# Performance work log

Hardware: AMD Instinct MI355X
Metric: run time of the kernel (lower is better)

## Reference

```python
import jax, jax.numpy as jnp
import numpy as np

EMB_DIM = 1024
HEAD_SIZE = 64
SEQ = 2048
BATCH = 8


def setup_inputs() -> dict:
    key = jax.random.key(0)
    kx, kq, kk, kv = jax.random.split(key, 4)
    x = jax.random.normal(kx, (BATCH, SEQ, EMB_DIM), dtype=jnp.float32)
    # nn.Linear(E, H, bias=False): y = x @ W.T with W of shape [H, E]; store as [E, H]
    s = 1.0 / np.sqrt(EMB_DIM)
    Wq = jax.random.uniform(kq, (EMB_DIM, HEAD_SIZE), jnp.float32, -s, s)
    Wk = jax.random.uniform(kk, (EMB_DIM, HEAD_SIZE), jnp.float32, -s, s)
    Wv = jax.random.uniform(kv, (EMB_DIM, HEAD_SIZE), jnp.float32, -s, s)
    return {"x": x, "Wq": Wq, "Wk": Wk, "Wv": Wv}


def reference(x, Wq, Wk, Wv):
    B, S, E = x.shape
    q = jnp.einsum("bse,eh->bsh", x, Wq)
    k = jnp.einsum("bse,eh->bsh", x, Wk)
    v = jnp.einsum("bse,eh->bsh", x, Wv)
    # NOTE: original scales by E**-0.5 (embedding dim), not head_size**-0.5
    att = jnp.einsum("bqh,bkh->bqk", q, k) * (E ** -0.5)
    causal = jnp.tril(jnp.ones((S, S), dtype=bool))
    att = jnp.where(causal, att, -jnp.inf)
    att = jax.nn.softmax(att, axis=-1)
    # dropout(p=0.2) treated as identity (eval mode) for deterministic reference
    out = jnp.einsum("bqk,bkh->bqh", att, v)
    return out
```

## Files before the change

kernel.cpp:

```cpp
#include <hip/hip_runtime.h>

constexpr int Bn = 8, S = 2048, E = 1024, H = 64;
constexpr float SCALE = 0.03125f;
constexpr float LOG2E = 1.44269504f;

typedef __attribute__((ext_vector_type(8))) short short8;
typedef __attribute__((ext_vector_type(4))) float f32x4;

__device__ __forceinline__ unsigned short f2bf(float f) {
  unsigned u = __builtin_bit_cast(unsigned, f);
  u += 0x7fffu + ((u >> 16) & 1u);
  return (unsigned short)(u >> 16);
}
__device__ __forceinline__ ushort4 f4bf(float4 f) {
  return make_ushort4(f2bf(f.x), f2bf(f.y), f2bf(f.z), f2bf(f.w));
}

__global__ __launch_bounds__(256) void wtrans_kernel(
    const float* __restrict__ Wq, const float* __restrict__ Wk,
    const float* __restrict__ Wv, unsigned short* __restrict__ WT3) {
  __shared__ unsigned short tb[64][72];
  const int m = blockIdx.x >> 4;
  const int e0 = (blockIdx.x & 15) * 64;
  const float* W = (m == 0) ? Wq : (m == 1) ? Wk : Wv;
  const int t = threadIdx.x;
#pragma unroll
  for (int it = 0; it < 4; ++it) {
    int idx = t + it * 256;
    int r = idx >> 4, c4 = idx & 15;
    float4 f = ((const float4*)(W + (long)(e0 + r) * H))[c4];
    *(ushort4*)&tb[r][c4 * 4] = f4bf(f);
  }
  __syncthreads();
#pragma unroll
  for (int it = 0; it < 4; ++it) {
    int idx = t + it * 256;
    int h = idx >> 4, e4 = idx & 15;
    ushort4 u = make_ushort4(tb[e4 * 4 + 0][h], tb[e4 * 4 + 1][h],
                             tb[e4 * 4 + 2][h], tb[e4 * 4 + 3][h]);
    ((ushort4*)(WT3 + (long)(m * 64 + h) * E + e0))[e4] = u;
  }
}

__global__ __launch_bounds__(256) void qkv_kernel(
    const float* __restrict__ x, const unsigned short* __restrict__ WT3,
    unsigned short* __restrict__ q, unsigned short* __restrict__ kk,
    unsigned short* __restrict__ vT) {
  __shared__ unsigned short xs[32][136];
  __shared__ unsigned short ws[192][136];
  const int t = threadIdx.x;
  const int w = t >> 6, lane = t & 63, l15 = lane & 15, g = lane >> 4;
  const long row0 = (long)blockIdx.x * 32;
  const int xrow = t >> 5, xslot = t & 31;
  const int wrow = t >> 4, wslot = t & 15;

  f32x4 acc[2][3];
#pragma unroll
  for (int rt = 0; rt < 2; ++rt)
#pragma unroll
    for (int ct = 0; ct < 3; ++ct) acc[rt][ct] = f32x4{0.f, 0.f, 0.f, 0.f};

  float4 px[4];
  short8 pw[12];
#pragma unroll
  for (int it = 0; it < 4; ++it)
    px[it] = ((const float4*)(x + (row0 + xrow + it * 8) * E))[xslot];
#pragma unroll
  for (int it = 0; it < 12; ++it)
    pw[it] = *(const short8*)(WT3 + (long)(wrow + it * 16) * E + wslot * 8);
#pragma unroll
  for (int it = 0; it < 4; ++it)
    *(ushort4*)&xs[xrow + it * 8][xslot * 4] = f4bf(px[it]);
#pragma unroll
  for (int it = 0; it < 12; ++it)
    *(short8*)&ws[wrow + it * 16][wslot * 8] = pw[it];

  for (int c = 0; c < 8; ++c) {
    __syncthreads();
    if (c < 7) {
      const int e0 = (c + 1) * 128;
#pragma unroll
      for (int it = 0; it < 4; ++it)
        px[it] = ((const float4*)(x + (row0 + xrow + it * 8) * E + e0))[xslot];
#pragma unroll
      for (int it = 0; it < 12; ++it)
        pw[it] = *(const short8*)(WT3 + (long)(wrow + it * 16) * E + e0 + wslot * 8);
    }
#pragma unroll
    for (int kh = 0; kh < 4; ++kh) {
      short8 a0 = *(const short8*)&xs[l15][kh * 32 + g * 8];
      short8 a1 = *(const short8*)&xs[16 + l15][kh * 32 + g * 8];
#pragma unroll
      for (int ct = 0; ct < 3; ++ct) {
        short8 b = *(const short8*)&ws[w * 48 + ct * 16 + l15][kh * 32 + g * 8];
        acc[0][ct] = __builtin_amdgcn_mfma_f32_16x16x32_bf16(a0, b, acc[0][ct], 0, 0, 0);
        acc[1][ct] = __builtin_amdgcn_mfma_f32_16x16x32_bf16(a1, b, acc[1][ct], 0, 0, 0);
      }
    }
    __syncthreads();
    if (c < 7) {
#pragma unroll
      for (int it = 0; it < 4; ++it)
        *(ushort4*)&xs[xrow + it * 8][xslot * 4] = f4bf(px[it]);
#pragma unroll
      for (int it = 0; it < 12; ++it)
        *(short8*)&ws[wrow + it * 16][wslot * 8] = pw[it];
    }
  }

  const int bb = (int)(row0 >> 11);
  const int srow = (int)(row0 & 2047);
#pragma unroll
  for (int ct = 0; ct < 3; ++ct) {
    const int col = w * 48 + ct * 16 + l15;
    const int mm = col >> 6, ch = col & 63;
#pragma unroll
    for (int rt = 0; rt < 2; ++rt) {
      const int srl = rt * 16 + g * 4;
      if (mm == 0) {
#pragma unroll
        for (int r = 0; r < 4; ++r)
          q[(row0 + srl + r) * H + ch] = f2bf(acc[rt][ct][r] * SCALE);
      } else if (mm == 1) {
#pragma unroll
        for (int r = 0; r < 4; ++r)
          kk[(row0 + srl + r) * H + ch] = f2bf(acc[rt][ct][r]);
      } else {
        ushort4 v4 = make_ushort4(f2bf(acc[rt][ct][0]), f2bf(acc[rt][ct][1]),
                                  f2bf(acc[rt][ct][2]), f2bf(acc[rt][ct][3]));
        *(ushort4*)(vT + ((long)bb * H + ch) * S + srow + srl) = v4;
      }
    }
  }
}

__global__ __launch_bounds__(256, 2) void attn_kernel(
    const unsigned short* __restrict__ q, const unsigned short* __restrict__ k,
    const unsigned short* __restrict__ vT, float* __restrict__ out) {
  __shared__ unsigned short pl[4][16][72];
  __shared__ float Om[2][64][20];
  __shared__ float ms[2][16], ls[2][16];
  const int t = threadIdx.x;
  const int w = t >> 6, lane = t & 63, l15 = lane & 15, g = lane >> 4;
  const int b = blockIdx.x & 7, p = blockIdx.x >> 3;
  const int grp = w >> 1, sp = w & 1;
  const int qt = grp ? (127 - p) : p;
  const int qrow0 = qt * 16;
  const int nt = (16 * qt + 79) >> 6;
  const unsigned short* kb = k + (long)b * S * H;
  const unsigned short* vb = vT + (long)b * H * S;
  const unsigned short* qp = q + ((long)b * S + qrow0 + l15) * H + g * 8;
  short8 bq0 = *(const short8*)qp;
  short8 bq1 = *(const short8*)(qp + 32);

  f32x4 O[4];
#pragma unroll
  for (int c = 0; c < 4; ++c) O[c] = f32x4{0.f, 0.f, 0.f, 0.f};
  float m_ = -1e30f, l_ = 0.f;

  short8 ak[4][2];
  int kt = sp;
  if (kt < nt) {
#pragma unroll
    for (int c = 0; c < 4; ++c)
#pragma unroll
      for (int kh = 0; kh < 2; ++kh)
        ak[c][kh] = *(const short8*)(kb + (long)(kt * 64 + c * 16 + l15) * H + kh * 32 + g * 8);
  }

  for (; kt < nt; kt += 2) {
    short8 av[4][2];
#pragma unroll
    for (int c = 0; c < 4; ++c)
#pragma unroll
      for (int kh = 0; kh < 2; ++kh)
        av[c][kh] = *(const short8*)(vb + (long)(c * 16 + l15) * S + kt * 64 + kh * 32 + g * 8);
    f32x4 sc[4];
#pragma unroll
    for (int c = 0; c < 4; ++c) {
      sc[c] = f32x4{0.f, 0.f, 0.f, 0.f};
      sc[c] = __builtin_amdgcn_mfma_f32_16x16x32_bf16(ak[c][0], bq0, sc[c], 0, 0, 0);
      sc[c] = __builtin_amdgcn_mfma_f32_16x16x32_bf16(ak[c][1], bq1, sc[c], 0, 0, 0);
    }
    if (kt + 2 < nt) {
#pragma unroll
      for (int c = 0; c < 4; ++c)
#pragma unroll
        for (int kh = 0; kh < 2; ++kh)
          ak[c][kh] = *(const short8*)(kb + (long)((kt + 2) * 64 + c * 16 + l15) * H + kh * 32 + g * 8);
    }
    if (kt == nt - 1) {
#pragma unroll
      for (int c = 0; c < 4; ++c)
#pragma unroll
        for (int r = 0; r < 4; ++r)
          if (kt * 64 + c * 16 + g * 4 + r > qrow0 + l15) sc[c][r] = -1e30f;
    }
    float mx = -1e30f;
#pragma unroll
    for (int c = 0; c < 4; ++c)
#pragma unroll
      for (int r = 0; r < 4; ++r) mx = fmaxf(mx, sc[c][r]);
    mx = fmaxf(mx, __shfl_xor(mx, 16));
    mx = fmaxf(mx, __shfl_xor(mx, 32));
    float mn = fmaxf(m_, mx);
    float al = exp2f((m_ - mn) * LOG2E);
    float sum = 0.f;
#pragma unroll
    for (int c = 0; c < 4; ++c)
#pragma unroll
      for (int r = 0; r < 4; ++r) {
        float pe = exp2f((sc[c][r] - mn) * LOG2E);
        sc[c][r] = pe;
        sum += pe;
      }
    sum += __shfl_xor(sum, 16);
    sum += __shfl_xor(sum, 32);
    l_ = l_ * al + sum;
    m_ = mn;
#pragma unroll
    for (int c = 0; c < 4; ++c) {
      ushort4 p4 = make_ushort4(f2bf(sc[c][0]), f2bf(sc[c][1]),
                                f2bf(sc[c][2]), f2bf(sc[c][3]));
      *(ushort4*)&pl[w][l15][c * 16 + g * 4] = p4;
    }
#pragma unroll
    for (int c = 0; c < 4; ++c)
#pragma unroll
      for (int r = 0; r < 4; ++r) O[c][r] *= al;
    short8 bp0 = *(const short8*)&pl[w][l15][g * 8];
    short8 bp1 = *(const short8*)&pl[w][l15][32 + g * 8];
#pragma unroll
    for (int c = 0; c < 4; ++c) {
      O[c] = __builtin_amdgcn_mfma_f32_16x16x32_bf16(av[c][0], bp0, O[c], 0, 0, 0);
      O[c] = __builtin_amdgcn_mfma_f32_16x16x32_bf16(av[c][1], bp1, O[c], 0, 0, 0);
    }
  }

  if (sp == 1) {
#pragma unroll
    for (int c = 0; c < 4; ++c)
#pragma unroll
      for (int r = 0; r < 4; ++r)
        Om[grp][c * 16 + g * 4 + r][l15] = O[c][r];
    if (g == 0) { ms[grp][l15] = m_; ls[grp][l15] = l_; }
  }
  __syncthreads();
  if (sp == 0) {
    float m1 = ms[grp][l15], l1 = ls[grp][l15];
    float mstar = fmaxf(m_, m1);
    float f0 = exp2f((m_ - mstar) * LOG2E);
    float f1 = exp2f((m1 - mstar) * LOG2E);
    float inv = 1.0f / (l_ * f0 + l1 * f1);
    float* op = out + ((long)b * S + qrow0 + l15) * H;
#pragma unroll
    for (int c = 0; c < 4; ++c) {
      float4 o;
      o.x = (O[c][0] * f0 + Om[grp][c * 16 + g * 4 + 0][l15] * f1) * inv;
      o.y = (O[c][1] * f0 + Om[grp][c * 16 + g * 4 + 1][l15] * f1) * inv;
      o.z = (O[c][2] * f0 + Om[grp][c * 16 + g * 4 + 2][l15] * f1) * inv;
      o.w = (O[c][3] * f0 + Om[grp][c * 16 + g * 4 + 3][l15] * f1) * inv;
      *(float4*)(op + c * 16 + g * 4) = o;
    }
  }
}

extern "C" void kernel_launch(void* const* d_in, const int* in_sizes, int n_in,
                              void* d_out, int out_size, void* d_ws, size_t ws_size,
                              hipStream_t stream) {
  const float* x  = (const float*)d_in[0];
  const float* Wq = (const float*)d_in[1];
  const float* Wk = (const float*)d_in[2];
  const float* Wv = (const float*)d_in[3];
  float* outp = (float*)d_out;
  unsigned short* WT3 = (unsigned short*)d_ws;
  unsigned short* q  = (unsigned short*)((char*)d_ws + 512 * 1024);
  unsigned short* kk = q + (size_t)Bn * S * H;
  unsigned short* vT = kk + (size_t)Bn * S * H;
  wtrans_kernel<<<dim3(48), dim3(256), 0, stream>>>(Wq, Wk, Wv, WT3);
  qkv_kernel<<<dim3((Bn * S) / 32), dim3(256), 0, stream>>>(x, WT3, q, kk, vT);
  attn_kernel<<<dim3(Bn * 64), dim3(256), 0, stream>>>(q, kk, vT, outp);
}
```

Before: 141.3 us.

## Split each attention block's key range across all four waves for both query tiles

Previously each block paired a short and a long query tile, with two waves per tile splitting key tiles in stride 2. Now all four waves process both query tiles in turn, striding key tiles by 4 with a rotated start offset so that work stays balanced across waves. The four partial softmax states are merged through larger shared-memory buffers. LOG2E is also folded into the Q scale so exp2 skips a multiply. This adds shared-memory traffic and a four-way merge, and keeps two sets of accumulators live, which raises register pressure.

```diff
diff --git a/kernel.cpp b/kernel.cpp
--- a/kernel.cpp
+++ b/kernel.cpp
@@ -1,8 +1,7 @@
 #include <hip/hip_runtime.h>
 
 constexpr int Bn = 8, S = 2048, E = 1024, H = 64;
-constexpr float SCALE = 0.03125f;
-constexpr float LOG2E = 1.44269504f;
+constexpr float SCALE = 0.03125f * 1.44269504f;
 
 typedef __attribute__((ext_vector_type(8))) short short8;
 typedef __attribute__((ext_vector_type(4))) float f32x4;
@@ -138,129 +137,148 @@
     const unsigned short* __restrict__ q, const unsigned short* __restrict__ k,
     const unsigned short* __restrict__ vT, float* __restrict__ out) {
   __shared__ unsigned short pl[4][16][72];
-  __shared__ float Om[2][64][20];
-  __shared__ float ms[2][16], ls[2][16];
+  __shared__ float Om[2][4][64][17];
+  __shared__ float ms[2][4][16], ls[2][4][16];
   const int t = threadIdx.x;
   const int w = t >> 6, lane = t & 63, l15 = lane & 15, g = lane >> 4;
   const int b = blockIdx.x & 7, p = blockIdx.x >> 3;
-  const int grp = w >> 1, sp = w & 1;
-  const int qt = grp ? (127 - p) : p;
-  const int qrow0 = qt * 16;
-  const int nt = (16 * qt + 79) >> 6;
   const unsigned short* kb = k + (long)b * S * H;
   const unsigned short* vb = vT + (long)b * H * S;
-  const unsigned short* qp = q + ((long)b * S + qrow0 + l15) * H + g * 8;
-  short8 bq0 = *(const short8*)qp;
-  short8 bq1 = *(const short8*)(qp + 32);
-
-  f32x4 O[4];
-#pragma unroll
-  for (int c = 0; c < 4; ++c) O[c] = f32x4{0.f, 0.f, 0.f, 0.f};
-  float m_ = -1e30f, l_ = 0.f;
-
-  short8 ak[4][2];
-  int kt = sp;
-  if (kt < nt) {
+
+  const int qt0 = p, qt1 = 127 - p;
+  const int nt0 = (qt0 >> 2) + 1;
+  const int nt1 = (qt1 >> 2) + 1;
+  const int qtA[2] = {qt0, qt1};
+  const int ntA[2] = {nt0, nt1};
+  const int k0A[2] = {w, (w + 4 - (nt0 & 3)) & 3};
+
+  short8 bq0[2], bq1[2];
+  f32x4 O[2][4];
+  float m_[2], l_[2];
+#pragma unroll
+  for (int ph = 0; ph < 2; ++ph) {
+    const unsigned short* qp = q + ((long)b * S + qtA[ph] * 16 + l15) * H + g * 8;
+    bq0[ph] = *(const short8*)qp;
+    bq1[ph] = *(const short8*)(qp + 32);
+    m_[ph] = -1e30f;
+    l_[ph] = 0.f;
+#pragma unroll
+    for (int c = 0; c < 4; ++c) O[ph][c] = f32x4{0.f, 0.f, 0.f, 0.f};
+  }
+
+#pragma unroll
+  for (int ph = 0; ph < 2; ++ph) {
+    const int qrow0 = qtA[ph] * 16;
+    const int ntp = ntA[ph];
+    short8 ak[4][2];
+    int kt = k0A[ph];
+    if (kt < ntp) {
+#pragma unroll
+      for (int c = 0; c < 4; ++c)
+#pragma unroll
+        for (int kh = 0; kh < 2; ++kh)
+          ak[c][kh] = *(const short8*)(kb + (long)(kt * 64 + c * 16 + l15) * H + kh * 32 + g * 8);
+    }
+    for (; kt < ntp; kt += 4) {
+      short8 av[4][2];
+#pragma unroll
+      for (int c = 0; c < 4; ++c)
+#pragma unroll
+        for (int kh = 0; kh < 2; ++kh)
+          av[c][kh] = *(const short8*)(vb + (long)(c * 16 + l15) * S + kt * 64 + kh * 32 + g * 8);
+      f32x4 sc[4];
+#pragma unroll
+      for (int c = 0; c < 4; ++c) {
+        sc[c] = f32x4{0.f, 0.f, 0.f, 0.f};
+        sc[c] = __builtin_amdgcn_mfma_f32_16x16x32_bf16(ak[c][0], bq0[ph], sc[c], 0, 0, 0);
+        sc[c] = __builtin_amdgcn_mfma_f32_16x16x32_bf16(ak[c][1], bq1[ph], sc[c], 0, 0, 0);
+      }
+      if (kt + 4 < ntp) {
+#pragma unroll
+        for (int c = 0; c < 4; ++c)
+#pragma unroll
+          for (int kh = 0; kh < 2; ++kh)
+            ak[c][kh] = *(const short8*)(kb + (long)((kt + 4) * 64 + c * 16 + l15) * H + kh * 32 + g * 8);
+      }
+      if (kt == ntp - 1) {
+#pragma unroll
+        for (int c = 0; c < 4; ++c)
+#pragma unroll
+          for (int r = 0; r < 4; ++r)
+            if (kt * 64 + c * 16 + g * 4 + r > qrow0 + l15) sc[c][r] = -1e30f;
+      }
+      float mx = -1e30f;
+#pragma unroll
+      for (int c = 0; c < 4; ++c)
+#pragma unroll
+        for (int r = 0; r < 4; ++r) mx = fmaxf(mx, sc[c][r]);
+      mx = fmaxf(mx, __shfl_xor(mx, 16));
+      mx = fmaxf(mx, __shfl_xor(mx, 32));
+      float mn = fmaxf(m_[ph], mx);
+      float al = exp2f(m_[ph] - mn);
+      float sum = 0.f;
+#pragma unroll
+      for (int c = 0; c < 4; ++c)
+#pragma unroll
+        for (int r = 0; r < 4; ++r) {
+          float pe = exp2f(sc[c][r] - mn);
+          sc[c][r] = pe;
+          sum += pe;
+        }
+      sum += __shfl_xor(sum, 16);
+      sum += __shfl_xor(sum, 32);
+      l_[ph] = l_[ph] * al + sum;
+      m_[ph] = mn;
+#pragma unroll
+      for (int c = 0; c < 4; ++c) {
+        ushort4 p4 = make_ushort4(f2bf(sc[c][0]), f2bf(sc[c][1]),
+                                  f2bf(sc[c][2]), f2bf(sc[c][3]));
+        *(ushort4*)&pl[w][l15][c * 16 + g * 4] = p4;
+      }
+#pragma unroll
+      for (int c = 0; c < 4; ++c)
+#pragma unroll
+        for (int r = 0; r < 4; ++r) O[ph][c][r] *= al;
+      short8 bp0 = *(const short8*)&pl[w][l15][g * 8];
+      short8 bp1 = *(const short8*)&pl[w][l15][32 + g * 8];
+#pragma unroll
+      for (int c = 0; c < 4; ++c) {
+        O[ph][c] = __builtin_amdgcn_mfma_f32_16x16x32_bf16(av[c][0], bp0, O[ph][c], 0, 0, 0);
+        O[ph][c] = __builtin_amdgcn_mfma_f32_16x16x32_bf16(av[c][1], bp1, O[ph][c], 0, 0, 0);
+      }
+    }
+  }
+
+#pragma unroll
+  for (int ph = 0; ph < 2; ++ph) {
 #pragma unroll
     for (int c = 0; c < 4; ++c)
 #pragma unroll
-      for (int kh = 0; kh < 2; ++kh)
-        ak[c][kh] = *(const short8*)(kb + (long)(kt * 64 + c * 16 + l15) * H + kh * 32 + g * 8);
-  }
-
-  for (; kt < nt; kt += 2) {
-    short8 av[4][2];
-#pragma unroll
-    for (int c = 0; c < 4; ++c)
-#pragma unroll
-      for (int kh = 0; kh < 2; ++kh)
-        av[c][kh] = *(const short8*)(vb + (long)(c * 16 + l15) * S + kt * 64 + kh * 32 + g * 8);
-    f32x4 sc[4];
+      for (int r = 0; r < 4; ++r)
+        Om[ph][w][c * 16 + g * 4 + r][l15] = O[ph][c][r];
+    if (g == 0) { ms[ph][w][l15] = m_[ph]; ls[ph][w][l15] = l_[ph]; }
+  }
+  __syncthreads();
+  if (w < 2) {
+    const int ph = w;
+    float mm0 = ms[ph][0][l15], mm1 = ms[ph][1][l15];
+    float mm2 = ms[ph][2][l15], mm3 = ms[ph][3][l15];
+    float mstar = fmaxf(fmaxf(mm0, mm1), fmaxf(mm2, mm3));
+    float f0 = exp2f(mm0 - mstar), f1 = exp2f(mm1 - mstar);
+    float f2 = exp2f(mm2 - mstar), f3 = exp2f(mm3 - mstar);
+    float inv = 1.0f / (ls[ph][0][l15] * f0 + ls[ph][1][l15] * f1 +
+                        ls[ph][2][l15] * f2 + ls[ph][3][l15] * f3);
+    float* op = out + ((long)b * S + qtA[ph] * 16 + l15) * H;
 #pragma unroll
     for (int c = 0; c < 4; ++c) {
-      sc[c] = f32x4{0.f, 0.f, 0.f, 0.f};
-      sc[c] = __builtin_amdgcn_mfma_f32_16x16x32_bf16(ak[c][0], bq0, sc[c], 0, 0, 0);
-      sc[c] = __builtin_amdgcn_mfma_f32_16x16x32_bf16(ak[c][1], bq1, sc[c], 0, 0, 0);
-    }
-    if (kt + 2 < nt) {
-#pragma unroll
-      for (int c = 0; c < 4; ++c)
-#pragma unroll
-        for (int kh = 0; kh < 2; ++kh)
-          ak[c][kh] = *(const short8*)(kb + (long)((kt + 2) * 64 + c * 16 + l15) * H + kh * 32 + g * 8);
-    }
-    if (kt == nt - 1) {
-#pragma unroll
-      for (int c = 0; c < 4; ++c)
-#pragma unroll
-        for (int r = 0; r < 4; ++r)
-          if (kt * 64 + c * 16 + g * 4 + r > qrow0 + l15) sc[c][r] = -1e30f;
-    }
-    float mx = -1e30f;
-#pragma unroll
-    for (int c = 0; c < 4; ++c)
-#pragma unroll
-      for (int r = 0; r < 4; ++r) mx = fmaxf(mx, sc[c][r]);
-    mx = fmaxf(mx, __shfl_xor(mx, 16));
-    mx = fmaxf(mx, __shfl_xor(mx, 32));
-    float mn = fmaxf(m_, mx);
-    float al = exp2f((m_ - mn) * LOG2E);
-    float sum = 0.f;
-#pragma unroll
-    for (int c = 0; c < 4; ++c)
+      float o4[4];
 #pragma unroll
       for (int r = 0; r < 4; ++r) {
-        float pe = exp2f((sc[c][r] - mn) * LOG2E);
-        sc[c][r] = pe;
-        sum += pe;
-      }
-    sum += __shfl_xor(sum, 16);
-    sum += __shfl_xor(sum, 32);
-    l_ = l_ * al + sum;
-    m_ = mn;
-#pragma unroll
-    for (int c = 0; c < 4; ++c) {
-      ushort4 p4 = make_ushort4(f2bf(sc[c][0]), f2bf(sc[c][1]),
-                                f2bf(sc[c][2]), f2bf(sc[c][3]));
-      *(ushort4*)&pl[w][l15][c * 16 + g * 4] = p4;
-    }
-#pragma unroll
-    for (int c = 0; c < 4; ++c)
-#pragma unroll
-      for (int r = 0; r < 4; ++r) O[c][r] *= al;
-    short8 bp0 = *(const short8*)&pl[w][l15][g * 8];
-    short8 bp1 = *(const short8*)&pl[w][l15][32 + g * 8];
-#pragma unroll
-    for (int c = 0; c < 4; ++c) {
-      O[c] = __builtin_amdgcn_mfma_f32_16x16x32_bf16(av[c][0], bp0, O[c], 0, 0, 0);
-      O[c] = __builtin_amdgcn_mfma_f32_16x16x32_bf16(av[c][1], bp1, O[c], 0, 0, 0);
-    }
-  }
-
-  if (sp == 1) {
-#pragma unroll
-    for (int c = 0; c < 4; ++c)
-#pragma unroll
-      for (int r = 0; r < 4; ++r)
-        Om[grp][c * 16 + g * 4 + r][l15] = O[c][r];
-    if (g == 0) { ms[grp][l15] = m_; ls[grp][l15] = l_; }
-  }
-  __syncthreads();
-  if (sp == 0) {
-    float m1 = ms[grp][l15], l1 = ls[grp][l15];
-    float mstar = fmaxf(m_, m1);
-    float f0 = exp2f((m_ - mstar) * LOG2E);
-    float f1 = exp2f((m1 - mstar) * LOG2E);
-    float inv = 1.0f / (l_ * f0 + l1 * f1);
-    float* op = out + ((long)b * S + qrow0 + l15) * H;
-#pragma unroll
-    for (int c = 0; c < 4; ++c) {
-      float4 o;
-      o.x = (O[c][0] * f0 + Om[grp][c * 16 + g * 4 + 0][l15] * f1) * inv;
-      o.y = (O[c][1] * f0 + Om[grp][c * 16 + g * 4 + 1][l15] * f1) * inv;
-      o.z = (O[c][2] * f0 + Om[grp][c * 16 + g * 4 + 2][l15] * f1) * inv;
-      o.w = (O[c][3] * f0 + Om[grp][c * 16 + g * 4 + 3][l15] * f1) * inv;
-      *(float4*)(op + c * 16 + g * 4) = o;
+        const int h = c * 16 + g * 4 + r;
+        o4[r] = (Om[ph][0][h][l15] * f0 + Om[ph][1][h][l15] * f1 +
+                 Om[ph][2][h][l15] * f2 + Om[ph][3][h][l15] * f3) * inv;
+      }
+      *(float4*)(op + c * 16 + g * 4) = make_float4(o4[0], o4[1], o4[2], o4[3]);
     }
   }
 }
```

Measured after the change: 141.4 us. Within noise of the previous version (+0.1%).

## Split each query tile's KV range across four waves and fold log2e into scale

Applied to the files above, without the earlier changes.

Each attention block previously handled two query tiles, with two waves splitting the key range of each. It now handles a single query tile whose key blocks are strided across all four waves, and the grid is doubled. The four partial softmax states are merged through shared memory in a cooperative epilogue. The log2e factor is folded into the Q scale so the exp2 calls need no extra multiply, and the max and sum reductions are rewritten as trees. The launch bound now targets four blocks per CU. The aim is more parallelism and shorter per-wave chains; the cost is a bigger merge and less per-block balancing between causal tiles.

```diff
diff --git a/kernel.cpp b/kernel.cpp
--- a/kernel.cpp
+++ b/kernel.cpp
@@ -1,8 +1,7 @@
 #include <hip/hip_runtime.h>
 
 constexpr int Bn = 8, S = 2048, E = 1024, H = 64;
-constexpr float SCALE = 0.03125f;
-constexpr float LOG2E = 1.44269504f;
+constexpr float SCALE = 0.03125f * 1.44269504f;
 
 typedef __attribute__((ext_vector_type(8))) short short8;
 typedef __attribute__((ext_vector_type(4))) float f32x4;
@@ -134,21 +133,21 @@
   }
 }
 
-__global__ __launch_bounds__(256, 2) void attn_kernel(
+__global__ __launch_bounds__(256, 4) void attn_kernel(
     const unsigned short* __restrict__ q, const unsigned short* __restrict__ k,
     const unsigned short* __restrict__ vT, float* __restrict__ out) {
   __shared__ unsigned short pl[4][16][72];
-  __shared__ float Om[2][64][20];
-  __shared__ float ms[2][16], ls[2][16];
+  __shared__ float Om[4][64][17];
+  __shared__ float ms[4][16], ls[4][16];
   const int t = threadIdx.x;
   const int w = t >> 6, lane = t & 63, l15 = lane & 15, g = lane >> 4;
   const int b = blockIdx.x & 7, p = blockIdx.x >> 3;
-  const int grp = w >> 1, sp = w & 1;
-  const int qt = grp ? (127 - p) : p;
+  const int qt = 127 - p;
   const int qrow0 = qt * 16;
-  const int nt = (16 * qt + 79) >> 6;
+  const int nt = (qt >> 2) + 1;
   const unsigned short* kb = k + (long)b * S * H;
   const unsigned short* vb = vT + (long)b * H * S;
+
   const unsigned short* qp = q + ((long)b * S + qrow0 + l15) * H + g * 8;
   short8 bq0 = *(const short8*)qp;
   short8 bq1 = *(const short8*)(qp + 32);
@@ -159,7 +158,7 @@
   float m_ = -1e30f, l_ = 0.f;
 
   short8 ak[4][2];
-  int kt = sp;
+  int kt = w;
   if (kt < nt) {
 #pragma unroll
     for (int c = 0; c < 4; ++c)
@@ -168,7 +167,7 @@
         ak[c][kh] = *(const short8*)(kb + (long)(kt * 64 + c * 16 + l15) * H + kh * 32 + g * 8);
   }
 
-  for (; kt < nt; kt += 2) {
+  for (; kt < nt; kt += 4) {
     short8 av[4][2];
 #pragma unroll
     for (int c = 0; c < 4; ++c)
@@ -182,12 +181,12 @@
       sc[c] = __builtin_amdgcn_mfma_f32_16x16x32_bf16(ak[c][0], bq0, sc[c], 0, 0, 0);
       sc[c] = __builtin_amdgcn_mfma_f32_16x16x32_bf16(ak[c][1], bq1, sc[c], 0, 0, 0);
     }
-    if (kt + 2 < nt) {
+    if (kt + 4 < nt) {
 #pragma unroll
       for (int c = 0; c < 4; ++c)
 #pragma unroll
         for (int kh = 0; kh < 2; ++kh)
-          ak[c][kh] = *(const short8*)(kb + (long)((kt + 2) * 64 + c * 16 + l15) * H + kh * 32 + g * 8);
+          ak[c][kh] = *(const short8*)(kb + (long)((kt + 4) * 64 + c * 16 + l15) * H + kh * 32 + g * 8);
     }
     if (kt == nt - 1) {
 #pragma unroll
@@ -196,24 +195,24 @@
         for (int r = 0; r < 4; ++r)
           if (kt * 64 + c * 16 + g * 4 + r > qrow0 + l15) sc[c][r] = -1e30f;
     }
-    float mx = -1e30f;
-#pragma unroll
-    for (int c = 0; c < 4; ++c)
-#pragma unroll
-      for (int r = 0; r < 4; ++r) mx = fmaxf(mx, sc[c][r]);
+    float x0 = fmaxf(fmaxf(sc[0][0], sc[0][1]), fmaxf(sc[0][2], sc[0][3]));
+    float x1 = fmaxf(fmaxf(sc[1][0], sc[1][1]), fmaxf(sc[1][2], sc[1][3]));
+    float x2 = fmaxf(fmaxf(sc[2][0], sc[2][1]), fmaxf(sc[2][2], sc[2][3]));
+    float x3 = fmaxf(fmaxf(sc[3][0], sc[3][1]), fmaxf(sc[3][2], sc[3][3]));
+    float mx = fmaxf(fmaxf(x0, x1), fmaxf(x2, x3));
     mx = fmaxf(mx, __shfl_xor(mx, 16));
     mx = fmaxf(mx, __shfl_xor(mx, 32));
     float mn = fmaxf(m_, mx);
-    float al = exp2f((m_ - mn) * LOG2E);
-    float sum = 0.f;
-#pragma unroll
-    for (int c = 0; c < 4; ++c)
-#pragma unroll
-      for (int r = 0; r < 4; ++r) {
-        float pe = exp2f((sc[c][r] - mn) * LOG2E);
-        sc[c][r] = pe;
-        sum += pe;
-      }
+    float al = exp2f(m_ - mn);
+#pragma unroll
+    for (int c = 0; c < 4; ++c)
+#pragma unroll
+      for (int r = 0; r < 4; ++r) sc[c][r] = exp2f(sc[c][r] - mn);
+    float s0 = (sc[0][0] + sc[0][1]) + (sc[0][2] + sc[0][3]);
+    float s1 = (sc[1][0] + sc[1][1]) + (sc[1][2] + sc[1][3]);
+    float s2 = (sc[2][0] + sc[2][1]) + (sc[2][2] + sc[2][3]);
+    float s3 = (sc[3][0] + sc[3][1]) + (sc[3][2] + sc[3][3]);
+    float sum = (s0 + s1) + (s2 + s3);
     sum += __shfl_xor(sum, 16);
     sum += __shfl_xor(sum, 32);
     l_ = l_ * al + sum;
@@ -237,31 +236,31 @@
     }
   }
 
-  if (sp == 1) {
-#pragma unroll
-    for (int c = 0; c < 4; ++c)
-#pragma unroll
-      for (int r = 0; r < 4; ++r)
-        Om[grp][c * 16 + g * 4 + r][l15] = O[c][r];
-    if (g == 0) { ms[grp][l15] = m_; ls[grp][l15] = l_; }
-  }
+  if (g == 0) { ms[w][l15] = m_; ls[w][l15] = l_; }
+#pragma unroll
+  for (int c = 0; c < 4; ++c)
+#pragma unroll
+    for (int r = 0; r < 4; ++r)
+      Om[w][c * 16 + g * 4 + r][l15] = O[c][r];
   __syncthreads();
-  if (sp == 0) {
-    float m1 = ms[grp][l15], l1 = ls[grp][l15];
-    float mstar = fmaxf(m_, m1);
-    float f0 = exp2f((m_ - mstar) * LOG2E);
-    float f1 = exp2f((m1 - mstar) * LOG2E);
-    float inv = 1.0f / (l_ * f0 + l1 * f1);
-    float* op = out + ((long)b * S + qrow0 + l15) * H;
-#pragma unroll
-    for (int c = 0; c < 4; ++c) {
-      float4 o;
-      o.x = (O[c][0] * f0 + Om[grp][c * 16 + g * 4 + 0][l15] * f1) * inv;
-      o.y = (O[c][1] * f0 + Om[grp][c * 16 + g * 4 + 1][l15] * f1) * inv;
-      o.z = (O[c][2] * f0 + Om[grp][c * 16 + g * 4 + 2][l15] * f1) * inv;
-      o.w = (O[c][3] * f0 + Om[grp][c * 16 + g * 4 + 3][l15] * f1) * inv;
-      *(float4*)(op + c * 16 + g * 4) = o;
-    }
+  {
+    const int row = t >> 4, h0 = (t & 15) * 4;
+    float m0 = ms[0][row], m1 = ms[1][row], m2 = ms[2][row], m3 = ms[3][row];
+    float mstar = fmaxf(fmaxf(m0, m1), fmaxf(m2, m3));
+    float f0 = exp2f(m0 - mstar), f1 = exp2f(m1 - mstar);
+    float f2 = exp2f(m2 - mstar), f3 = exp2f(m3 - mstar);
+    float inv = 1.0f / (ls[0][row] * f0 + ls[1][row] * f1 +
+                        ls[2][row] * f2 + ls[3][row] * f3);
+    float4 o;
+    o.x = (Om[0][h0 + 0][row] * f0 + Om[1][h0 + 0][row] * f1 +
+           Om[2][h0 + 0][row] * f2 + Om[3][h0 + 0][row] * f3) * inv;
+    o.y = (Om[0][h0 + 1][row] * f0 + Om[1][h0 + 1][row] * f1 +
+           Om[2][h0 + 1][row] * f2 + Om[3][h0 + 1][row] * f3) * inv;
+    o.z = (Om[0][h0 + 2][row] * f0 + Om[1][h0 + 2][row] * f1 +
+           Om[2][h0 + 2][row] * f2 + Om[3][h0 + 2][row] * f3) * inv;
+    o.w = (Om[0][h0 + 3][row] * f0 + Om[1][h0 + 3][row] * f1 +
+           Om[2][h0 + 3][row] * f2 + Om[3][h0 + 3][row] * f3) * inv;
+    *(float4*)(out + ((long)b * S + qrow0 + row) * H + h0) = o;
   }
 }
 
@@ -279,5 +278,5 @@
   unsigned short* vT = kk + (size_t)Bn * S * H;
   wtrans_kernel<<<dim3(48), dim3(256), 0, stream>>>(Wq, Wk, Wv, WT3);
   qkv_kernel<<<dim3((Bn * S) / 32), dim3(256), 0, stream>>>(x, WT3, q, kk, vT);
-  attn_kernel<<<dim3(Bn * 64), dim3(256), 0, stream>>>(q, kk, vT, outp);
-}
+  attn_kernel<<<dim3(Bn * 128), dim3(256), 0, stream>>>(q, kk, vT, outp);
+}
```

Result: slower. 153.3 us (+8.5%).
